# Optimization experiments

Hardware: AMD Instinct MI355X
Metric: run time of the kernel (lower is better)

Reference implementation:

```python
import jax, jax.numpy as jnp
import numpy as np


def _bilinear_translate(img, tx, ty):
    """Translate a single [H,W] image by (tx, ty) pixels (tfa.image.translate
    convention: out(y, x) = in(y - ty, x - tx)), bilinear sampling, 0 fill."""
    H, W = img.shape
    ys = jnp.arange(H, dtype=img.dtype)[:, None] - ty  # [H,1] source rows
    xs = jnp.arange(W, dtype=img.dtype)[None, :] - tx  # [1,W] source cols
    y0f = jnp.floor(ys)
    x0f = jnp.floor(xs)
    wy = ys - y0f  # [H,1] fractional weights
    wx = xs - x0f  # [1,W]
    y0 = y0f.astype(jnp.int32)
    x0 = x0f.astype(jnp.int32)

    def corner(yi, xi):
        valid = (yi >= 0) & (yi <= H - 1) & (xi >= 0) & (xi <= W - 1)  # [H,W]
        v = img[jnp.clip(yi, 0, H - 1), jnp.clip(xi, 0, W - 1)]       # [H,W]
        return jnp.where(valid, v, jnp.zeros((), img.dtype))

    c00 = corner(y0, x0)
    c01 = corner(y0, x0 + 1)
    c10 = corner(y0 + 1, x0)
    c11 = corner(y0 + 1, x0 + 1)
    return ((1 - wy) * ((1 - wx) * c00 + wx * c01)
            + wy * ((1 - wx) * c10 + wx * c11))


def setup_inputs() -> dict:
    key = jax.random.key(0)
    k1, k2, k3 = jax.random.split(key, 3)
    B, T, H, W = 16, 64, 256, 256
    images = jax.random.normal(k1, (B, T, H, W), dtype=jnp.float32)
    dx = jax.random.normal(k2, (B, T), dtype=jnp.float32)  # subpixel shifts
    dy = jax.random.normal(k3, (B, T), dtype=jnp.float32)
    winsize = 256  # tiled in original call() but unused by translate_image
    return {"images": images, "dx": dx, "dy": dy, "winsize": winsize}


def reference(images, dx, dy, winsize):
    B, T, H, W = images.shape
    flat = images.reshape(B * T, H, W)
    out = jax.vmap(_bilinear_translate)(flat, dx.reshape(-1), dy.reshape(-1))
    return out.reshape(B, T, H, W)
```

## Files before the change

kernel.cpp:

```cpp
#include <hip/hip_runtime.h>


constexpr int HH = 256;
constexpr int WW = 256;

__global__ __launch_bounds__(256) void translate_kernel(
    const float* __restrict__ img,
    const float* __restrict__ dx,
    const float* __restrict__ dy,
    float* __restrict__ out)
{
    const int n = blockIdx.x >> 8;
    const int y = blockIdx.x & 255;
    const int x = threadIdx.x;

    const float tx = dx[n];
    const float ty = dy[n];

    const float ysf = (float)y - ty;
    const float xsf = (float)x - tx;
    const float y0f = floorf(ysf);
    const float x0f = floorf(xsf);
    const float wy  = ysf - y0f;
    const float wx  = xsf - x0f;
    const int y0 = (int)y0f;
    const int x0 = (int)x0f;
    const int y1 = y0 + 1;
    const int x1 = x0 + 1;

    const bool vy0 = (y0 >= 0) && (y0 < HH);
    const bool vy1 = (y1 >= 0) && (y1 < HH);
    const bool vx0 = (x0 >= 0) && (x0 < WW);
    const bool vx1 = (x1 >= 0) && (x1 < WW);

    const int yc0 = min(max(y0, 0), HH - 1);
    const int yc1 = min(max(y1, 0), HH - 1);
    const int xc0 = min(max(x0, 0), WW - 1);
    const int xc1 = min(max(x1, 0), WW - 1);

    const float* base = img + (size_t)n * (HH * WW);
    const float* row0 = base + yc0 * WW;
    const float* row1 = base + yc1 * WW;

    const float c00 = (vy0 && vx0) ? row0[xc0] : 0.0f;
    const float c01 = (vy0 && vx1) ? row0[xc1] : 0.0f;
    const float c10 = (vy1 && vx0) ? row1[xc0] : 0.0f;
    const float c11 = (vy1 && vx1) ? row1[xc1] : 0.0f;

    const float top = (1.0f - wx) * c00 + wx * c01;
    const float bot = (1.0f - wx) * c10 + wx * c11;
    const float r   = (1.0f - wy) * top + wy * bot;

    out[((size_t)n * HH + y) * WW + x] = r;
}

extern "C" void kernel_launch(void* const* d_in, const int* in_sizes, int n_in,
                              void* d_out, int out_size, void* d_ws, size_t ws_size,
                              hipStream_t stream) {
    const float* img = (const float*)d_in[0];
    const float* dx  = (const float*)d_in[1];
    const float* dy  = (const float*)d_in[2];
    float* out = (float*)d_out;

    const int BT = in_sizes[1];
    const int nblocks = BT * HH;

    translate_kernel<<<nblocks, WW, 0, stream>>>(img, dx, dy, out);
}
```

Baseline: 500.2 us.

## Stage row band in LDS with float4 loads and compute 16 rows per block

Each block now handles a 16-row band of one image. It cooperatively loads the needed source rows (band plus halo) into shared memory with float4 vector loads, zero-filling rows that fall out of range, then computes bilinear samples from LDS. This removes the redundant global reads of neighbouring rows and the per-pixel scattered loads, and cuts the block count. The cost is an extra barrier and LDS traffic. It relies on the shift being small enough that the rows touched fit in 18 rows.

```diff
diff --git a/kernel.cpp b/kernel.cpp
--- a/kernel.cpp
+++ b/kernel.cpp
@@ -3,6 +3,8 @@
 
 constexpr int HH = 256;
 constexpr int WW = 256;
+constexpr int RB = 16;
+constexpr int SROWS = RB + 2;
 
 __global__ __launch_bounds__(256) void translate_kernel(
     const float* __restrict__ img,
@@ -10,48 +12,75 @@
     const float* __restrict__ dy,
     float* __restrict__ out)
 {
-    const int n = blockIdx.x >> 8;
-    const int y = blockIdx.x & 255;
-    const int x = threadIdx.x;
+    __shared__ float lds[SROWS][WW];
+
+    const int n  = blockIdx.x >> 4;
+    const int yb = (blockIdx.x & 15) * RB;
 
     const float tx = dx[n];
     const float ty = dy[n];
 
-    const float ysf = (float)y - ty;
-    const float xsf = (float)x - tx;
-    const float y0f = floorf(ysf);
-    const float x0f = floorf(xsf);
-    const float wy  = ysf - y0f;
-    const float wx  = xsf - x0f;
-    const int y0 = (int)y0f;
-    const int x0 = (int)x0f;
-    const int y1 = y0 + 1;
-    const int x1 = x0 + 1;
+    const int rmin = (int)floorf((float)yb - ty);
+    const int rmax = (int)floorf((float)(yb + RB - 1) - ty) + 1;
+    const int nrows = rmax - rmin + 1;
 
-    const bool vy0 = (y0 >= 0) && (y0 < HH);
-    const bool vy1 = (y1 >= 0) && (y1 < HH);
-    const bool vx0 = (x0 >= 0) && (x0 < WW);
-    const bool vx1 = (x1 >= 0) && (x1 < WW);
+    const int tid = threadIdx.x;
+    {
+        const float4* __restrict__ img4 =
+            (const float4*)(img + (size_t)n * (HH * WW));
+        float4* lds4 = (float4*)&lds[0][0];
+        const int total = nrows * (WW / 4);
+        for (int idx = tid; idx < total; idx += 256) {
+            const int rr   = idx >> 6;
+            const int cc   = idx & 63;
+            const int srow = rmin + rr;
+            float4 v = make_float4(0.f, 0.f, 0.f, 0.f);
+            if ((unsigned)srow < (unsigned)HH)
+                v = img4[srow * (WW / 4) + cc];
+            lds4[idx] = v;
+        }
+    }
+    __syncthreads();
 
-    const int yc0 = min(max(y0, 0), HH - 1);
-    const int yc1 = min(max(y1, 0), HH - 1);
-    const int xc0 = min(max(x0, 0), WW - 1);
-    const int xc1 = min(max(x1, 0), WW - 1);
+    const int lane = tid & 63;
+    const int wv   = tid >> 6;
 
-    const float* base = img + (size_t)n * (HH * WW);
-    const float* row0 = base + yc0 * WW;
-    const float* row1 = base + yc1 * WW;
+    #pragma unroll
+    for (int jr = 0; jr < 4; ++jr) {
+        const int r = (wv << 2) | jr;
+        const int y = yb + r;
 
-    const float c00 = (vy0 && vx0) ? row0[xc0] : 0.0f;
-    const float c01 = (vy0 && vx1) ? row0[xc1] : 0.0f;
-    const float c10 = (vy1 && vx0) ? row1[xc0] : 0.0f;
-    const float c11 = (vy1 && vx1) ? row1[xc1] : 0.0f;
+        const float ysf = (float)y - ty;
+        const float y0f = floorf(ysf);
+        const float wy  = ysf - y0f;
+        const int   ly0 = (int)y0f - rmin;
+        const float* __restrict__ L0 = &lds[ly0][0];
+        const float* __restrict__ L1 = &lds[ly0 + 1][0];
+        float* __restrict__ orow = out + ((size_t)n * HH + y) * WW;
 
-    const float top = (1.0f - wx) * c00 + wx * c01;
-    const float bot = (1.0f - wx) * c10 + wx * c11;
-    const float r   = (1.0f - wy) * top + wy * bot;
+        #pragma unroll
+        for (int k = 0; k < 4; ++k) {
+            const int x = (k << 6) | lane;
+            const float xsf = (float)x - tx;
+            const float x0f = floorf(xsf);
+            const float wx  = xsf - x0f;
+            const int x0 = (int)x0f;
+            const int x1 = x0 + 1;
+            const bool vx0 = ((unsigned)x0 < (unsigned)WW);
+            const bool vx1 = ((unsigned)x1 < (unsigned)WW);
+            const int xc0 = min(max(x0, 0), WW - 1);
+            const int xc1 = min(max(x1, 0), WW - 1);
 
-    out[((size_t)n * HH + y) * WW + x] = r;
+            const float c00 = vx0 ? L0[xc0] : 0.0f;
+            const float c01 = vx1 ? L0[xc1] : 0.0f;
+            const float c10 = vx0 ? L1[xc0] : 0.0f;
+            const float c11 = vx1 ? L1[xc1] : 0.0f;
+
+            const float top = (1.0f - wx) * c00 + wx * c01;
+            const float bot = (1.0f - wx) * c10 + wx * c11;
+            orow[x] = (1.0f - wy) * top + wy * bot;
+        }
+    }
 }
 
 extern "C" void kernel_launch(void* const* d_in, const int* in_sizes, int n_in,
@@ -63,7 +92,7 @@
     float* out = (float*)d_out;
 
     const int BT = in_sizes[1];
-    const int nblocks = BT * HH;
+    const int nblocks = BT * (HH / RB);
 
-    translate_kernel<<<nblocks, WW, 0, stream>>>(img, dx, dy, out);
+    translate_kernel<<<nblocks, 256, 0, stream>>>(img, dx, dy, out);
 }
```

Result: faster. 432.6 us (-13.5%).
